# Optimization experiments

Measured on AMD Instinct MI355X. Metric: run time of the kernel, lower is better.

The kernel has to match this reference:

```python
import jax, jax.numpy as jnp
import numpy as np

B, R, N, F = 16, 13, 392, 256
POOL_CH = 512
NB_CLASSES = 200
ALPHA = 0.5
BN_EPS = 1e-3


def gcn_norm_ones(n):
    # GCNConv.preprocess on an all-ones adjacency: A_hat = A + I, D = (n+1)I,
    # D^-1/2 A_hat D^-1/2 = (ones + eye) / (n + 1)
    return (jnp.ones((n, n), jnp.float32) + jnp.eye(n, dtype=jnp.float32)) / (n + 1.0)


def appnp(x, A, w, b, alpha):
    # Spektral APPNPConv, no hidden layers, mlp_activation='sigmoid', propagations=1
    h = jax.nn.sigmoid(x @ w + b)
    return (1.0 - alpha) * jnp.einsum('mn,...nf->...mf', A, h) + alpha * h


def gat_dense(x, A, kernel, attn_s, attn_n, bias):
    # Faithful translation of the modified GATConv._call_dense
    xk = jnp.einsum('...ni,iho->...nho', x, kernel)            # [..., N, H, Fo]
    s = jnp.einsum('...nhi,iho->...nho', xk, attn_s)           # [..., N, H, 1]
    nb = jnp.einsum('...nhi,iho->...nho', xk, attn_n)          # [..., N, H, 1]
    nb = jnp.einsum('...abc->...cba', nb)                      # [..., 1, H, N]
    coef = jax.nn.leaky_relu(s + nb, 0.2)                      # [..., N, H, N]
    # add_self_loops then mask where a == 0 (normalized ones adjacency -> no masking)
    a = A.at[jnp.arange(A.shape[-1]), jnp.arange(A.shape[-1])].set(1.0)
    mask = jnp.where(a == 0.0, -1e10, 0.0).astype(coef.dtype)  # [N, N]
    coef = coef + mask[:, None, :]
    coef = jax.nn.softmax(coef, axis=-1)
    out = jnp.einsum('...nhm,...mhi->...nhi', coef, xk)        # [..., N, H, Fo]
    out = out.reshape(out.shape[:-2] + (-1,)) + bias           # concat heads
    return jax.nn.elu(out)


def setup_inputs() -> dict:
    key = jax.random.key(0)
    ks = jax.random.split(key, 8)
    s = lambda k, shape, sc: (jax.random.normal(k, shape, jnp.float32) * sc)
    return {
        'x': s(ks[0], (B, R, N, F), 1.0),
        'w_mlp': s(ks[1], (F, F), F ** -0.5),
        'b_mlp': jnp.zeros((F,), jnp.float32),
        'k_gat': s(ks[2], (F, 1, F), F ** -0.5),
        'a_self': s(ks[3], (F, 1, 1), F ** -0.5),
        'a_neigh': s(ks[4], (F, 1, 1), F ** -0.5),
        'b_gat': jnp.zeros((F,), jnp.float32),
        'wf_pool': s(ks[5], (F, POOL_CH), F ** -0.5),
        'bf_pool': jnp.zeros((POOL_CH,), jnp.float32),
        'wa_pool': s(ks[6], (F, POOL_CH), F ** -0.5),
        'ba_pool': jnp.zeros((POOL_CH,), jnp.float32),
        'bn_gamma': jnp.ones((POOL_CH,), jnp.float32),
        'bn_beta': jnp.zeros((POOL_CH,), jnp.float32),
        'bn_mean': jnp.zeros((POOL_CH,), jnp.float32),
        'bn_var': jnp.ones((POOL_CH,), jnp.float32),
        'w_out': s(ks[7], (POOL_CH, NB_CLASSES), POOL_CH ** -0.5),
        'b_out': jnp.zeros((NB_CLASSES,), jnp.float32),
    }


def reference(x, w_mlp, b_mlp, k_gat, a_self, a_neigh, b_gat,
              wf_pool, bf_pool, wa_pool, ba_pool,
              bn_gamma, bn_beta, bn_mean, bn_var, w_out, b_out):
    A_intra = gcn_norm_ones(N)   # [N, N]
    A_inter = gcn_norm_ones(R)   # [R, R]

    # Intra-ROI: APPNP + residual, GAT + residual (all R graphs share weights/adj)
    h = appnp(x, A_intra, w_mlp, b_mlp, ALPHA) + x                      # [B,R,N,F]
    x2_intra = gat_dense(h, A_intra, k_gat, a_self, a_neigh, b_gat) + h
    x2_intra = x2_intra.reshape(x.shape[0], R * N, F)

    # Inter-ROI: transpose so ROIs are the graph nodes
    xt = jnp.transpose(x, (0, 2, 1, 3))                                 # [B,N,R,F]
    h2 = appnp(xt, A_inter, w_mlp, b_mlp, ALPHA) + xt
    x2_inter = gat_dense(h2, A_inter, k_gat, a_self, a_neigh, b_gat) + h2
    x2_inter = x2_inter.reshape(x.shape[0], N * R, F)

    x2 = jnp.concatenate([x2_intra, x2_inter], axis=1)                  # [B, 2RN, F]

    # GlobalAttentionPool(512)
    attn = jax.nn.sigmoid(x2 @ wa_pool + ba_pool)
    feat = x2 @ wf_pool + bf_pool
    pooled = jnp.sum(attn * feat, axis=1)                               # [B, 512]

    # BatchNorm (inference) + softmax classifier
    bn = (pooled - bn_mean) * jax.lax.rsqrt(bn_var + BN_EPS) * bn_gamma + bn_beta
    return jax.nn.softmax(bn @ w_out + b_out, axis=-1)
```

## Files before the change

### kernel.cpp

```cpp
#include <hip/hip_runtime.h>
#include <hip/hip_bf16.h>

#define B_    16
#define R_    13
#define N_    392
#define F_    256
#define RN_   (R_*N_)
#define M_    (B_*RN_)
#define POOL_ 512
#define NCLS_ 200

typedef __attribute__((ext_vector_type(4))) float f32x4;
typedef __attribute__((ext_vector_type(8))) short bf16x8;
typedef __attribute__((ext_vector_type(8))) unsigned short u16x8;

__device__ __forceinline__ unsigned short f2b(float f){
  union { float f; unsigned u; } v; v.f = f;
  unsigned r = v.u + 0x7FFF + ((v.u >> 16) & 1);
  return (unsigned short)(r >> 16);
}
__device__ __forceinline__ float b2f(unsigned short b){
  union { unsigned u; float f; } v; v.u = ((unsigned)b) << 16;
  return v.f;
}

__device__ __forceinline__ float warpMax(float v){
  #pragma unroll
  for (int o = 32; o; o >>= 1) v = fmaxf(v, __shfl_down(v, o));
  return v;
}
__device__ __forceinline__ float warpSum(float v){
  #pragma unroll
  for (int o = 32; o; o >>= 1) v += __shfl_down(v, o);
  return v;
}
__device__ __forceinline__ float blockMax(float v, float* red){
  v = warpMax(v);
  __syncthreads();
  if ((threadIdx.x & 63) == 0) red[threadIdx.x >> 6] = v;
  __syncthreads();
  return fmaxf(fmaxf(red[0], red[1]), fmaxf(red[2], red[3]));
}
__device__ __forceinline__ float blockSum(float v, float* red){
  v = warpSum(v);
  __syncthreads();
  if ((threadIdx.x & 63) == 0) red[threadIdx.x >> 6] = v;
  __syncthreads();
  return red[0] + red[1] + red[2] + red[3];
}
__device__ __forceinline__ float eluf(float v){
  return v > 0.f ? v : (expf(v) - 1.f);
}

__global__ __launch_bounds__(256) void cvt_wt(const float* __restrict__ W,
    unsigned short* __restrict__ Wt, int K, int N){
  const int id = blockIdx.x*256 + threadIdx.x;
  if (id < K*N){
    const int n = id / K, k = id - n*K;
    Wt[id] = f2b(W[k*N + n]);
  }
}

__global__ __launch_bounds__(256) void cvt_x(const float* __restrict__ x,
    unsigned short* __restrict__ xb){
  const long t = (long)blockIdx.x*256 + threadIdx.x;
  const float4 a = *(const float4*)&x[t*8];
  const float4 b = *(const float4*)&x[t*8 + 4];
  u16x8 o = {f2b(a.x),f2b(a.y),f2b(a.z),f2b(a.w),f2b(b.x),f2b(b.y),f2b(b.z),f2b(b.w)};
  *(u16x8*)&xb[t*8] = o;
}

__global__ __launch_bounds__(256) void cvt_xT(const float* __restrict__ x,
    unsigned short* __restrict__ xb){
  const long t = (long)blockIdx.x*256 + threadIdx.x;
  const int l  = (int)(t >> 5);
  const int c8 = ((int)t & 31) * 8;
  const int b  = l / RN_;
  const int rem = l - b*RN_;
  const int n  = rem / R_;
  const int r  = rem - n*R_;
  const long prow = (long)(b*R_ + r)*N_ + n;
  const float4 a  = *(const float4*)&x[prow*F_ + c8];
  const float4 bb = *(const float4*)&x[prow*F_ + c8 + 4];
  u16x8 o = {f2b(a.x),f2b(a.y),f2b(a.z),f2b(a.w),f2b(bb.x),f2b(bb.y),f2b(bb.z),f2b(bb.w)};
  *(u16x8*)&xb[(long)l*F_ + c8] = o;
}

template<int ACT>
__global__ __launch_bounds__(256) void mfma_gemm(
    const unsigned short* __restrict__ A, const unsigned short* __restrict__ Wt,
    const float* __restrict__ bias, unsigned short* __restrict__ out){
  __shared__ unsigned short A_lds[128][72];
  __shared__ unsigned short W_lds[64][72];
  const int tid = threadIdx.x;
  const int lane = tid & 63, wid = tid >> 6;
  const int wr = wid >> 1, wc = wid & 1;
  const int lr = lane & 15, lk = lane >> 4;
  const int row0 = blockIdx.x * 128;
  const int col0 = blockIdx.y * 64;

  f32x4 acc[4][2] = {};
  for (int k0 = 0; k0 < 256; k0 += 64){
    #pragma unroll
    for (int i = 0; i < 4; ++i){
      const int chunk = tid + i*256;
      const int r = chunk >> 3, c8 = (chunk & 7)*8;
      *(u16x8*)&A_lds[r][c8] = *(const u16x8*)&A[(long)(row0 + r)*F_ + k0 + c8];
    }
    #pragma unroll
    for (int i = 0; i < 2; ++i){
      const int chunk = tid + i*256;
      const int r = chunk >> 3, c8 = (chunk & 7)*8;
      *(u16x8*)&W_lds[r][c8] = *(const u16x8*)&Wt[(long)(col0 + r)*F_ + k0 + c8];
    }
    __syncthreads();
    #pragma unroll
    for (int kk = 0; kk < 64; kk += 32){
      bf16x8 af[4], bf[2];
      #pragma unroll
      for (int m = 0; m < 4; ++m)
        af[m] = *(const bf16x8*)&A_lds[wr*64 + m*16 + lr][kk + lk*8];
      #pragma unroll
      for (int n = 0; n < 2; ++n)
        bf[n] = *(const bf16x8*)&W_lds[wc*32 + n*16 + lr][kk + lk*8];
      #pragma unroll
      for (int m = 0; m < 4; ++m)
        #pragma unroll
        for (int n = 0; n < 2; ++n)
          acc[m][n] = __builtin_amdgcn_mfma_f32_16x16x32_bf16(af[m], bf[n], acc[m][n], 0, 0, 0);
    }
    __syncthreads();
  }
  #pragma unroll
  for (int m = 0; m < 4; ++m){
    const int gr = row0 + wr*64 + m*16 + lk*4;
    #pragma unroll
    for (int n = 0; n < 2; ++n){
      const int gc = col0 + wc*32 + n*16 + lr;
      #pragma unroll
      for (int q = 0; q < 4; ++q){
        float v = acc[m][n][q];
        if (ACT) v = 1.f/(1.f + expf(-(v + bias[gc])));
        out[(long)(gr + q)*F_ + gc] = f2b(v);
      }
    }
  }
}

__global__ __launch_bounds__(256) void colsum_k(const unsigned short* __restrict__ h1,
    float* __restrict__ S, int nn){
  const int g = blockIdx.x;
  const int f = threadIdx.x;
  const unsigned short* base = h1 + (long)g*nn*F_ + f;
  float s = 0.f;
  for (int n = 0; n < nn; ++n) s += b2f(base[(long)n*F_]);
  S[(long)g*F_ + f] = s;
}

template<int XMODE>
__global__ __launch_bounds__(256) void combine_k(const unsigned short* __restrict__ h1,
    const float* __restrict__ S, const float* __restrict__ x,
    float* __restrict__ h, unsigned short* __restrict__ hb){
  const long t = (long)blockIdx.x*256 + threadIdx.x;
  const long row = t >> 6;
  const int f4 = ((int)t & 63) * 4;
  int g, xrow;
  if (XMODE == 0){ g = (int)(row / N_); xrow = (int)row; }
  else {
    g = (int)(row / R_);
    const int b   = (int)(row / RN_);
    const int rem = (int)(row - (long)b*RN_);
    const int n   = rem / R_;
    const int r   = rem - n*R_;
    xrow = (b*R_ + r)*N_ + n;
  }
  const float inv = (XMODE == 0) ? (1.f/(N_+1)) : (1.f/(R_+1));
  const ushort4 hraw = *(const ushort4*)&h1[row*F_ + f4];
  const float4 h1v = {b2f(hraw.x), b2f(hraw.y), b2f(hraw.z), b2f(hraw.w)};
  const float4 Sv  = *(const float4*)&S[(long)g*F_ + f4];
  const float4 xv  = *(const float4*)&x[(long)xrow*F_ + f4];
  float4 o;
  o.x = 0.5f*(Sv.x + h1v.x)*inv + 0.5f*h1v.x + xv.x;
  o.y = 0.5f*(Sv.y + h1v.y)*inv + 0.5f*h1v.y + xv.y;
  o.z = 0.5f*(Sv.z + h1v.z)*inv + 0.5f*h1v.z + xv.z;
  o.w = 0.5f*(Sv.w + h1v.w)*inv + 0.5f*h1v.w + xv.w;
  *(float4*)&h[row*F_ + f4] = o;
  const ushort4 ob = {f2b(o.x), f2b(o.y), f2b(o.z), f2b(o.w)};
  *(ushort4*)&hb[row*F_ + f4] = ob;
}

__global__ __launch_bounds__(256) void st_k(const unsigned short* __restrict__ xk,
    const float* __restrict__ a_self, const float* __restrict__ a_neigh,
    float* __restrict__ sv, float* __restrict__ tv){
  const int lane = threadIdx.x & 63;
  const int wid  = threadIdx.x >> 6;
  const long row = (long)blockIdx.x*4 + wid;
  const ushort4 raw = *(const ushort4*)&xk[row*F_ + lane*4];
  const float4 v  = {b2f(raw.x), b2f(raw.y), b2f(raw.z), b2f(raw.w)};
  const float4 as = *(const float4*)&a_self[lane*4];
  const float4 an = *(const float4*)&a_neigh[lane*4];
  float s = v.x*as.x + v.y*as.y + v.z*as.z + v.w*as.w;
  float t = v.x*an.x + v.y*an.y + v.z*an.z + v.w*an.w;
  #pragma unroll
  for (int o = 32; o; o >>= 1){ s += __shfl_down(s, o); t += __shfl_down(t, o); }
  if (lane == 0){ sv[row] = s; tv[row] = t; }
}

__global__ __launch_bounds__(256) void attn_intra_k(
    const unsigned short* __restrict__ xk, const float* __restrict__ sv,
    const float* __restrict__ tv, const float* __restrict__ bg,
    const float* __restrict__ h, unsigned short* __restrict__ x2){
  const int g  = blockIdx.y;
  const int m0 = blockIdx.x * 32;
  const int tid = threadIdx.x;
  __shared__ float t_lds[N_];
  __shared__ float w_lds[32][N_];
  __shared__ float invr[32];
  __shared__ float red[4];

  for (int n = tid; n < N_; n += 256) t_lds[n] = tv[(long)g*N_ + n];
  __syncthreads();
  float tl = -1e30f;
  for (int n = tid; n < N_; n += 256) tl = fmaxf(tl, t_lds[n]);
  const float tmax = blockMax(tl, red);

  const int nrows = min(32, N_ - m0);
  for (int j = 0; j < nrows; ++j){
    const float sm = sv[(long)g*N_ + m0 + j];
    float zm = sm + tmax; zm = zm > 0.f ? zm : 0.2f*zm;
    float loc = 0.f;
    for (int n = tid; n < N_; n += 256){
      float z = sm + t_lds[n];
      z = z > 0.f ? z : 0.2f*z;
      const float e = expf(z - zm);
      w_lds[j][n] = e;
      loc += e;
    }
    const float tot = blockSum(loc, red);
    if (tid == 0) invr[j] = 1.f / tot;
  }
  __syncthreads();

  const int ty = tid >> 6, tx = tid & 63;
  float4 acc[8];
  #pragma unroll
  for (int j = 0; j < 8; ++j) acc[j] = make_float4(0.f,0.f,0.f,0.f);
  const unsigned short* xkg = xk + (long)g*N_*F_;
  for (int n = 0; n < N_; ++n){
    const ushort4 raw = *(const ushort4*)&xkg[n*F_ + tx*4];
    const float4 xv = {b2f(raw.x), b2f(raw.y), b2f(raw.z), b2f(raw.w)};
    #pragma unroll
    for (int j = 0; j < 8; ++j){
      const float w = w_lds[ty*8 + j][n];
      acc[j].x += w*xv.x; acc[j].y += w*xv.y; acc[j].z += w*xv.z; acc[j].w += w*xv.w;
    }
  }
  const float4 bgv = *(const float4*)&bg[tx*4];
  #pragma unroll
  for (int j = 0; j < 8; ++j){
    const int m = m0 + ty*8 + j;
    if (m < N_){
      const float iv = invr[ty*8 + j];
      const long row = (long)g*N_ + m;
      const float4 hv = *(const float4*)&h[row*F_ + tx*4];
      ushort4 o;
      o.x = f2b(eluf(acc[j].x*iv + bgv.x) + hv.x);
      o.y = f2b(eluf(acc[j].y*iv + bgv.y) + hv.y);
      o.z = f2b(eluf(acc[j].z*iv + bgv.z) + hv.z);
      o.w = f2b(eluf(acc[j].w*iv + bgv.w) + hv.w);
      *(ushort4*)&x2[row*F_ + tx*4] = o;
    }
  }
}

__global__ __launch_bounds__(256) void attn_inter_k(
    const unsigned short* __restrict__ xk, const float* __restrict__ sv,
    const float* __restrict__ tv, const float* __restrict__ bg,
    const float* __restrict__ h, unsigned short* __restrict__ x2){
  const int g = blockIdx.x;
  const int tid = threadIdx.x;
  __shared__ float w_lds[R_][R_];
  __shared__ float invr[R_];
  __shared__ float st[R_], tt[R_];
  if (tid < R_){ st[tid] = sv[(long)g*R_ + tid]; tt[tid] = tv[(long)g*R_ + tid]; }
  __syncthreads();
  if (tid < R_){
    const float sm = st[tid];
    float z[R_];
    float zm = -1e30f;
    #pragma unroll
    for (int n = 0; n < R_; ++n){
      float zz = sm + tt[n];
      zz = zz > 0.f ? zz : 0.2f*zz;
      z[n] = zz;
      zm = fmaxf(zm, zz);
    }
    float sum = 0.f;
    #pragma unroll
    for (int n = 0; n < R_; ++n){
      const float e = expf(z[n] - zm);
      w_lds[tid][n] = e;
      sum += e;
    }
    invr[tid] = 1.f/sum;
  }
  __syncthreads();
  float acc[R_] = {};
  const unsigned short* xkg = xk + (long)g*R_*F_;
  #pragma unroll
  for (int n = 0; n < R_; ++n){
    const float xv = b2f(xkg[n*F_ + tid]);
    #pragma unroll
    for (int m = 0; m < R_; ++m) acc[m] += w_lds[m][n]*xv;
  }
  const float bgv = bg[tid];
  #pragma unroll
  for (int m = 0; m < R_; ++m){
    const long row = (long)g*R_ + m;
    const float hv = h[row*F_ + tid];
    x2[row*F_ + tid] = f2b(eluf(acc[m]*invr[m] + bgv) + hv);
  }
}

__global__ __launch_bounds__(256) void pool_mfma(
    const unsigned short* __restrict__ x2, const unsigned short* __restrict__ wat,
    const unsigned short* __restrict__ wft, const float* __restrict__ ba,
    const float* __restrict__ bfp, float* __restrict__ pooled){
  __shared__ unsigned short A_lds[128][72];
  __shared__ unsigned short Wa_lds[64][72];
  __shared__ unsigned short Wf_lds[64][72];
  __shared__ float redp[8][64];
  const int tid = threadIdx.x;
  const int lane = tid & 63, wid = tid >> 6;
  const int wr = wid >> 1, wc = wid & 1;
  const int lr = lane & 15, lk = lane >> 4;
  const int j0 = blockIdx.x * 128;
  const int c0 = blockIdx.y * 64;
  const int b  = blockIdx.z;
  const unsigned short* xb = x2 + (long)b * RN_ * F_;

  f32x4 accA[4][2] = {}, accF[4][2] = {};
  for (int k0 = 0; k0 < 256; k0 += 64){
    #pragma unroll
    for (int i = 0; i < 4; ++i){
      const int chunk = tid + i*256;
      const int r = chunk >> 3, c8 = (chunk & 7)*8;
      u16x8 v = {};
      if (j0 + r < RN_) v = *(const u16x8*)&xb[(long)(j0 + r)*F_ + k0 + c8];
      *(u16x8*)&A_lds[r][c8] = v;
    }
    #pragma unroll
    for (int i = 0; i < 2; ++i){
      const int chunk = tid + i*256;
      const int r = chunk >> 3, c8 = (chunk & 7)*8;
      *(u16x8*)&Wa_lds[r][c8] = *(const u16x8*)&wat[(long)(c0 + r)*F_ + k0 + c8];
      *(u16x8*)&Wf_lds[r][c8] = *(const u16x8*)&wft[(long)(c0 + r)*F_ + k0 + c8];
    }
    __syncthreads();
    #pragma unroll
    for (int kk = 0; kk < 64; kk += 32){
      bf16x8 af[4], bfa[2], bff[2];
      #pragma unroll
      for (int m = 0; m < 4; ++m)
        af[m] = *(const bf16x8*)&A_lds[wr*64 + m*16 + lr][kk + lk*8];
      #pragma unroll
      for (int n = 0; n < 2; ++n){
        bfa[n] = *(const bf16x8*)&Wa_lds[wc*32 + n*16 + lr][kk + lk*8];
        bff[n] = *(const bf16x8*)&Wf_lds[wc*32 + n*16 + lr][kk + lk*8];
      }
      #pragma unroll
      for (int m = 0; m < 4; ++m)
        #pragma unroll
        for (int n = 0; n < 2; ++n){
          accA[m][n] = __builtin_amdgcn_mfma_f32_16x16x32_bf16(af[m], bfa[n], accA[m][n], 0, 0, 0);
          accF[m][n] = __builtin_amdgcn_mfma_f32_16x16x32_bf16(af[m], bff[n], accF[m][n], 0, 0, 0);
        }
    }
    __syncthreads();
  }
  float csum[2] = {0.f, 0.f};
  #pragma unroll
  for (int m = 0; m < 4; ++m){
    const int jb = wr*64 + m*16 + lk*4;
    #pragma unroll
    for (int q = 0; q < 4; ++q){
      if (j0 + jb + q < RN_){
        #pragma unroll
        for (int n = 0; n < 2; ++n){
          const int c = c0 + wc*32 + n*16 + lr;
          const float a = accA[m][n][q] + ba[c];
          const float f = accF[m][n][q] + bfp[c];
          csum[n] += f / (1.f + expf(-a));
        }
      }
    }
  }
  #pragma unroll
  for (int n = 0; n < 2; ++n) redp[wr*4 + lk][wc*32 + n*16 + lr] = csum[n];
  __syncthreads();
  if (tid < 64){
    float s = 0.f;
    #pragma unroll
    for (int i = 0; i < 8; ++i) s += redp[i][tid];
    atomicAdd(&pooled[(long)b*POOL_ + c0 + tid], s);
  }
}

__global__ __launch_bounds__(256) void final_k(const float* __restrict__ pooled,
    const float* __restrict__ gamma, const float* __restrict__ beta,
    const float* __restrict__ mean, const float* __restrict__ var,
    const float* __restrict__ wout, const float* __restrict__ bout,
    float* __restrict__ out){
  const int b = blockIdx.x, tid = threadIdx.x;
  __shared__ float bn[POOL_];
  __shared__ float red[4];
  for (int c = tid; c < POOL_; c += 256){
    const float p = pooled[(long)b*POOL_ + c];
    bn[c] = (p - mean[c]) * rsqrtf(var[c] + 1e-3f) * gamma[c] + beta[c];
  }
  __syncthreads();
  float logit = -3.0e38f;
  if (tid < NCLS_){
    float s = bout[tid];
    for (int k = 0; k < POOL_; ++k) s += bn[k]*wout[k*NCLS_ + tid];
    logit = s;
  }
  const float mx = blockMax(logit, red);
  float e = (tid < NCLS_) ? expf(logit - mx) : 0.f;
  const float tot = blockSum(e, red);
  if (tid < NCLS_) out[(long)b*NCLS_ + tid] = e / tot;
}

extern "C" void kernel_launch(void* const* d_in, const int* in_sizes, int n_in,
                              void* d_out, int out_size, void* d_ws, size_t ws_size,
                              hipStream_t stream){
  const float* x       = (const float*)d_in[0];
  const float* w_mlp   = (const float*)d_in[1];
  const float* b_mlp   = (const float*)d_in[2];
  const float* k_gat   = (const float*)d_in[3];
  const float* a_self  = (const float*)d_in[4];
  const float* a_neigh = (const float*)d_in[5];
  const float* b_gat   = (const float*)d_in[6];
  const float* wf_pool = (const float*)d_in[7];
  const float* bf_pool = (const float*)d_in[8];
  const float* wa_pool = (const float*)d_in[9];
  const float* ba_pool = (const float*)d_in[10];
  const float* bn_g    = (const float*)d_in[11];
  const float* bn_b    = (const float*)d_in[12];
  const float* bn_m    = (const float*)d_in[13];
  const float* bn_v    = (const float*)d_in[14];
  const float* w_out   = (const float*)d_in[15];
  const float* b_out   = (const float*)d_in[16];
  float* out = (float*)d_out;

  char* p = (char*)d_ws;
  const long MF = (long)M_ * F_;
  unsigned short* abuf = (unsigned short*)p;  p += MF*2;
  float*          hbuf = (float*)p;           p += MF*4;
  unsigned short* xbuf = (unsigned short*)p;  p += MF*2;
  unsigned short* wmt  = (unsigned short*)p;  p += 65536*2;
  unsigned short* kgt  = (unsigned short*)p;  p += 65536*2;
  unsigned short* wat  = (unsigned short*)p;  p += 131072*2;
  unsigned short* wft  = (unsigned short*)p;  p += 131072*2;
  float*          Sbuf = (float*)p;           p += (long)B_*N_*F_*4;
  float*          sbuf = (float*)p;           p += (long)M_*4;
  float*          tbuf = (float*)p;           p += (long)M_*4;
  float*          pooled = (float*)p;         p += (long)B_*POOL_*4;

  hipMemsetAsync(pooled, 0, (size_t)B_*POOL_*sizeof(float), stream);

  cvt_wt<<<256, 256, 0, stream>>>(w_mlp,   wmt, 256, 256);
  cvt_wt<<<256, 256, 0, stream>>>(k_gat,   kgt, 256, 256);
  cvt_wt<<<512, 256, 0, stream>>>(wa_pool, wat, 256, 512);
  cvt_wt<<<512, 256, 0, stream>>>(wf_pool, wft, 256, 512);

  const dim3 ggrid(M_/128, F_/64);
  const dim3 pgrid((RN_+127)/128, POOL_/64, B_);

  cvt_x<<<M_*F_/2048, 256, 0, stream>>>(x, xbuf);
  mfma_gemm<1><<<ggrid, 256, 0, stream>>>(xbuf, wmt, b_mlp, abuf);
  colsum_k<<<B_*R_, 256, 0, stream>>>(abuf, Sbuf, N_);
  combine_k<0><<<M_*64/256, 256, 0, stream>>>(abuf, Sbuf, x, hbuf, xbuf);
  mfma_gemm<0><<<ggrid, 256, 0, stream>>>(xbuf, kgt, nullptr, abuf);
  st_k<<<M_/4, 256, 0, stream>>>(abuf, a_self, a_neigh, sbuf, tbuf);
  attn_intra_k<<<dim3(13, B_*R_), 256, 0, stream>>>(abuf, sbuf, tbuf, b_gat, hbuf, xbuf);
  pool_mfma<<<pgrid, 256, 0, stream>>>(xbuf, wat, wft, ba_pool, bf_pool, pooled);

  cvt_xT<<<M_*F_/2048, 256, 0, stream>>>(x, xbuf);
  mfma_gemm<1><<<ggrid, 256, 0, stream>>>(xbuf, wmt, b_mlp, abuf);
  colsum_k<<<B_*N_, 256, 0, stream>>>(abuf, Sbuf, R_);
  combine_k<1><<<M_*64/256, 256, 0, stream>>>(abuf, Sbuf, x, hbuf, xbuf);
  mfma_gemm<0><<<ggrid, 256, 0, stream>>>(xbuf, kgt, nullptr, abuf);
  st_k<<<M_/4, 256, 0, stream>>>(abuf, a_self, a_neigh, sbuf, tbuf);
  attn_inter_k<<<B_*N_, 256, 0, stream>>>(abuf, sbuf, tbuf, b_gat, hbuf, xbuf);
  pool_mfma<<<pgrid, 256, 0, stream>>>(xbuf, wat, wft, ba_pool, bf_pool, pooled);

  final_k<<<B_, 256, 0, stream>>>(pooled, bn_g, bn_b, bn_m, bn_v, w_out, b_out, out);
}
```

Before: 1.128 ms.

## Move intra-ROI attention aggregation to bf16 MFMA and drop fp32 h buffer

The intra-ROI attention weights are now computed per wave, stored as bf16 in LDS with a padded K dimension, and multiplied against a transposed xk by MFMA instead of scalar fp32 FMAs. A new transpose kernel produces the padded xkT layout. The fp32 residual buffer h is removed: the residual is read back from the bf16 hb buffer and the output is written in place. This trades extra rounding of the attention weights and residual for far less ALU work and memory traffic.

```diff
diff --git a/kernel.cpp b/kernel.cpp
--- a/kernel.cpp
+++ b/kernel.cpp
@@ -9,6 +9,8 @@
 #define M_    (B_*RN_)
 #define POOL_ 512
 #define NCLS_ 200
+#define KP_   416
+#define WPS_  424
 
 typedef __attribute__((ext_vector_type(4))) float f32x4;
 typedef __attribute__((ext_vector_type(8))) short bf16x8;
@@ -147,6 +149,28 @@
   }
 }
 
+__global__ __launch_bounds__(256) void xkT_k(const unsigned short* __restrict__ xk,
+    unsigned short* __restrict__ xkT){
+  __shared__ unsigned short tile[32][36];
+  const int n0 = blockIdx.x * 32;
+  const int f0 = blockIdx.y * 32;
+  const int g  = blockIdx.z;
+  const int t  = threadIdx.x;
+  {
+    const int nl = t >> 3, fl = (t & 7)*4;
+    ushort4 v = {0,0,0,0};
+    const int n = n0 + nl;
+    if (n < N_) v = *(const ushort4*)&xk[((long)g*N_ + n)*F_ + f0 + fl];
+    tile[nl][fl] = v.x; tile[nl][fl+1] = v.y; tile[nl][fl+2] = v.z; tile[nl][fl+3] = v.w;
+  }
+  __syncthreads();
+  {
+    const int fl = t >> 3, nl = (t & 7)*4;
+    ushort4 o = {tile[nl][fl], tile[nl+1][fl], tile[nl+2][fl], tile[nl+3][fl]};
+    *(ushort4*)&xkT[((long)g*F_ + f0 + fl)*KP_ + n0 + nl] = o;
+  }
+}
+
 __global__ __launch_bounds__(256) void colsum_k(const unsigned short* __restrict__ h1,
     float* __restrict__ S, int nn){
   const int g = blockIdx.x;
@@ -160,7 +184,7 @@
 template<int XMODE>
 __global__ __launch_bounds__(256) void combine_k(const unsigned short* __restrict__ h1,
     const float* __restrict__ S, const float* __restrict__ x,
-    float* __restrict__ h, unsigned short* __restrict__ hb){
+    unsigned short* __restrict__ hb){
   const long t = (long)blockIdx.x*256 + threadIdx.x;
   const long row = t >> 6;
   const int f4 = ((int)t & 63) * 4;
@@ -184,7 +208,6 @@
   o.y = 0.5f*(Sv.y + h1v.y)*inv + 0.5f*h1v.y + xv.y;
   o.z = 0.5f*(Sv.z + h1v.z)*inv + 0.5f*h1v.z + xv.z;
   o.w = 0.5f*(Sv.w + h1v.w)*inv + 0.5f*h1v.w + xv.w;
-  *(float4*)&h[row*F_ + f4] = o;
   const ushort4 ob = {f2b(o.x), f2b(o.y), f2b(o.z), f2b(o.w)};
   *(ushort4*)&hb[row*F_ + f4] = ob;
 }
@@ -207,68 +230,81 @@
 }
 
 __global__ __launch_bounds__(256) void attn_intra_k(
-    const unsigned short* __restrict__ xk, const float* __restrict__ sv,
+    const unsigned short* __restrict__ xkT, const float* __restrict__ sv,
     const float* __restrict__ tv, const float* __restrict__ bg,
-    const float* __restrict__ h, unsigned short* __restrict__ x2){
+    unsigned short* __restrict__ hx2){
+  __shared__ unsigned short Wp[64][WPS_];
+  __shared__ float t_lds[N_];
+  __shared__ float s_lds[64];
+  __shared__ float invr[64];
+  __shared__ float red[4];
   const int g  = blockIdx.y;
-  const int m0 = blockIdx.x * 32;
+  const int m0 = blockIdx.x * 64;
   const int tid = threadIdx.x;
-  __shared__ float t_lds[N_];
-  __shared__ float w_lds[32][N_];
-  __shared__ float invr[32];
-  __shared__ float red[4];
+  const int lane = tid & 63, wid = tid >> 6;
 
   for (int n = tid; n < N_; n += 256) t_lds[n] = tv[(long)g*N_ + n];
+  if (tid < 64) s_lds[tid] = (m0 + tid < N_) ? sv[(long)g*N_ + m0 + tid] : 0.f;
   __syncthreads();
   float tl = -1e30f;
   for (int n = tid; n < N_; n += 256) tl = fmaxf(tl, t_lds[n]);
   const float tmax = blockMax(tl, red);
 
-  const int nrows = min(32, N_ - m0);
-  for (int j = 0; j < nrows; ++j){
-    const float sm = sv[(long)g*N_ + m0 + j];
+  for (int j = 0; j < 16; ++j){
+    const int row = wid*16 + j;
+    const float sm = s_lds[row];
     float zm = sm + tmax; zm = zm > 0.f ? zm : 0.2f*zm;
     float loc = 0.f;
-    for (int n = tid; n < N_; n += 256){
-      float z = sm + t_lds[n];
-      z = z > 0.f ? z : 0.2f*z;
-      const float e = expf(z - zm);
-      w_lds[j][n] = e;
-      loc += e;
-    }
-    const float tot = blockSum(loc, red);
-    if (tid == 0) invr[j] = 1.f / tot;
-  }
-  __syncthreads();
-
-  const int ty = tid >> 6, tx = tid & 63;
-  float4 acc[8];
-  #pragma unroll
-  for (int j = 0; j < 8; ++j) acc[j] = make_float4(0.f,0.f,0.f,0.f);
-  const unsigned short* xkg = xk + (long)g*N_*F_;
-  for (int n = 0; n < N_; ++n){
-    const ushort4 raw = *(const ushort4*)&xkg[n*F_ + tx*4];
-    const float4 xv = {b2f(raw.x), b2f(raw.y), b2f(raw.z), b2f(raw.w)};
-    #pragma unroll
-    for (int j = 0; j < 8; ++j){
-      const float w = w_lds[ty*8 + j][n];
-      acc[j].x += w*xv.x; acc[j].y += w*xv.y; acc[j].z += w*xv.z; acc[j].w += w*xv.w;
-    }
-  }
-  const float4 bgv = *(const float4*)&bg[tx*4];
-  #pragma unroll
-  for (int j = 0; j < 8; ++j){
-    const int m = m0 + ty*8 + j;
-    if (m < N_){
-      const float iv = invr[ty*8 + j];
-      const long row = (long)g*N_ + m;
-      const float4 hv = *(const float4*)&h[row*F_ + tx*4];
-      ushort4 o;
-      o.x = f2b(eluf(acc[j].x*iv + bgv.x) + hv.x);
-      o.y = f2b(eluf(acc[j].y*iv + bgv.y) + hv.y);
-      o.z = f2b(eluf(acc[j].z*iv + bgv.z) + hv.z);
-      o.w = f2b(eluf(acc[j].w*iv + bgv.w) + hv.w);
-      *(ushort4*)&x2[row*F_ + tx*4] = o;
+    for (int n = lane; n < KP_; n += 64){
+      float e = 0.f;
+      if (n < N_){
+        float z = sm + t_lds[n];
+        z = z > 0.f ? z : 0.2f*z;
+        e = expf(z - zm);
+        loc += e;
+      }
+      Wp[row][n] = f2b(e);
+    }
+    loc = warpSum(loc);
+    if (lane == 0) invr[row] = 1.f / loc;
+  }
+  __syncthreads();
+
+  const int lr = lane & 15, lk = lane >> 4;
+  const int c0w = wid * 64;
+  const unsigned short* xkTg = xkT + (long)g*F_*KP_;
+  f32x4 acc[4][4] = {};
+  for (int ks = 0; ks < 13; ++ks){
+    const int k0 = ks*32;
+    bf16x8 af[4], bfr[4];
+    #pragma unroll
+    for (int mi = 0; mi < 4; ++mi)
+      af[mi] = *(const bf16x8*)&Wp[mi*16 + lr][k0 + lk*8];
+    #pragma unroll
+    for (int ni = 0; ni < 4; ++ni)
+      bfr[ni] = *(const bf16x8*)&xkTg[(long)(c0w + ni*16 + lr)*KP_ + k0 + lk*8];
+    #pragma unroll
+    for (int mi = 0; mi < 4; ++mi)
+      #pragma unroll
+      for (int ni = 0; ni < 4; ++ni)
+        acc[mi][ni] = __builtin_amdgcn_mfma_f32_16x16x32_bf16(af[mi], bfr[ni], acc[mi][ni], 0, 0, 0);
+  }
+  #pragma unroll
+  for (int mi = 0; mi < 4; ++mi){
+    #pragma unroll
+    for (int q = 0; q < 4; ++q){
+      const int lm = mi*16 + lk*4 + q;
+      const int m = m0 + lm;
+      if (m < N_){
+        const float iv = invr[lm];
+        #pragma unroll
+        for (int ni = 0; ni < 4; ++ni){
+          const int f = c0w + ni*16 + lr;
+          const long idx = ((long)g*N_ + m)*F_ + f;
+          const float v = eluf(acc[mi][ni][q]*iv + bg[f]) + b2f(hx2[idx]);
+          hx2[idx] = f2b(v);
+        }
+      }
     }
   }
 }
@@ -276,7 +312,7 @@
 __global__ __launch_bounds__(256) void attn_inter_k(
     const unsigned short* __restrict__ xk, const float* __restrict__ sv,
     const float* __restrict__ tv, const float* __restrict__ bg,
-    const float* __restrict__ h, unsigned short* __restrict__ x2){
+    unsigned short* __restrict__ hx2){
   const int g = blockIdx.x;
   const int tid = threadIdx.x;
   __shared__ float w_lds[R_][R_];
@@ -316,9 +352,9 @@
   const float bgv = bg[tid];
   #pragma unroll
   for (int m = 0; m < R_; ++m){
-    const long row = (long)g*R_ + m;
-    const float hv = h[row*F_ + tid];
-    x2[row*F_ + tid] = f2b(eluf(acc[m]*invr[m] + bgv) + hv);
+    const long idx = ((long)g*R_ + m)*F_ + tid;
+    const float hv = b2f(hx2[idx]);
+    hx2[idx] = f2b(eluf(acc[m]*invr[m] + bgv) + hv);
   }
 }
 
@@ -456,8 +492,8 @@
   char* p = (char*)d_ws;
   const long MF = (long)M_ * F_;
   unsigned short* abuf = (unsigned short*)p;  p += MF*2;
-  float*          hbuf = (float*)p;           p += MF*4;
   unsigned short* xbuf = (unsigned short*)p;  p += MF*2;
+  unsigned short* xkT  = (unsigned short*)p;  p += (long)B_*R_*F_*KP_*2;
   unsigned short* wmt  = (unsigned short*)p;  p += 65536*2;
   unsigned short* kgt  = (unsigned short*)p;  p += 65536*2;
   unsigned short* wat  = (unsigned short*)p;  p += 131072*2;
@@ -480,19 +516,20 @@
   cvt_x<<<M_*F_/2048, 256, 0, stream>>>(x, xbuf);
   mfma_gemm<1><<<ggrid, 256, 0, stream>>>(xbuf, wmt, b_mlp, abuf);
   colsum_k<<<B_*R_, 256, 0, stream>>>(abuf, Sbuf, N_);
-  combine_k<0><<<M_*64/256, 256, 0, stream>>>(abuf, Sbuf, x, hbuf, xbuf);
+  combine_k<0><<<M_*64/256, 256, 0, stream>>>(abuf, Sbuf, x, xbuf);
   mfma_gemm<0><<<ggrid, 256, 0, stream>>>(xbuf, kgt, nullptr, abuf);
+  xkT_k<<<dim3(KP_/32, F_/32, B_*R_), 256, 0, stream>>>(abuf, xkT);
   st_k<<<M_/4, 256, 0, stream>>>(abuf, a_self, a_neigh, sbuf, tbuf);
-  attn_intra_k<<<dim3(13, B_*R_), 256, 0, stream>>>(abuf, sbuf, tbuf, b_gat, hbuf, xbuf);
+  attn_intra_k<<<dim3(7, B_*R_), 256, 0, stream>>>(xkT, sbuf, tbuf, b_gat, xbuf);
   pool_mfma<<<pgrid, 256, 0, stream>>>(xbuf, wat, wft, ba_pool, bf_pool, pooled);
 
   cvt_xT<<<M_*F_/2048, 256, 0, stream>>>(x, xbuf);
   mfma_gemm<1><<<ggrid, 256, 0, stream>>>(xbuf, wmt, b_mlp, abuf);
   colsum_k<<<B_*N_, 256, 0, stream>>>(abuf, Sbuf, R_);
-  combine_k<1><<<M_*64/256, 256, 0, stream>>>(abuf, Sbuf, x, hbuf, xbuf);
+  combine_k<1><<<M_*64/256, 256, 0, stream>>>(abuf, Sbuf, x, xbuf);
   mfma_gemm<0><<<ggrid, 256, 0, stream>>>(xbuf, kgt, nullptr, abuf);
   st_k<<<M_/4, 256, 0, stream>>>(abuf, a_self, a_neigh, sbuf, tbuf);
-  attn_inter_k<<<B_*N_, 256, 0, stream>>>(abuf, sbuf, tbuf, b_gat, hbuf, xbuf);
+  attn_inter_k<<<B_*N_, 256, 0, stream>>>(abuf, sbuf, tbuf, b_gat, xbuf);
   pool_mfma<<<pgrid, 256, 0, stream>>>(xbuf, wat, wft, ba_pool, bf_pool, pooled);
 
   final_k<<<B_, 256, 0, stream>>>(pooled, bn_g, bn_b, bn_m, bn_v, w_out, b_out, out);
```

Result: faster. 959.5 us (-14.9%).
